# Optimization experiments

Hardware: AMD Instinct MI355X
Metric: run time of the kernel (lower is better)

## Reference

```python
import jax, jax.numpy as jnp
import numpy as np

ALPHA = 1.5
BETA = 0.5
AVG_RATIO = 1.0
SUM_TIMESTEPS = 28000
RANK = 8
K_TOP = RANK * RANK  # k = weight_1_a.shape[1] * weight_2_a.shape[1]


def setup_inputs() -> dict:
    key = jax.random.key(0)
    ks = jax.random.split(key, 5)
    B, S, D_IN, D_OUT = 2, 4096, 4096, 4096
    return {
        "hidden_states": jax.random.normal(ks[0], (B, S, D_IN), dtype=jnp.float32),
        "weight_1_a": jax.random.normal(ks[1], (D_OUT, RANK), dtype=jnp.float32) * 0.02,
        "weight_1_b": jax.random.normal(ks[2], (RANK, D_IN), dtype=jnp.float32) * 0.02,
        "weight_2_a": jax.random.normal(ks[3], (D_OUT, RANK), dtype=jnp.float32) * 0.02,
        "weight_2_b": jax.random.normal(ks[4], (RANK, D_IN), dtype=jnp.float32) * 0.02,
        "timestep": 1,
    }


def reference(hidden_states, weight_1_a, weight_1_b, weight_2_a, weight_2_b, timestep):
    # Low-rank expansions: [out, rank] @ [rank, in] -> [out, in]
    matrix1 = weight_1_a @ weight_1_b
    matrix2 = weight_2_a @ weight_2_b
    top_k_sum1 = jax.lax.top_k(jnp.abs(matrix1).ravel(), K_TOP)[0].sum()
    top_k_sum2 = jax.lax.top_k(jnp.abs(matrix2).ravel(), K_TOP)[0].sum()
    time_ratio = timestep % SUM_TIMESTEPS
    scale = (ALPHA * time_ratio / SUM_TIMESTEPS + BETA) % ALPHA  # pattern 's*'
    temp_ratio = (top_k_sum1 / AVG_RATIO) / (top_k_sum2 * scale)
    weight = jnp.where(temp_ratio > 1.0, matrix1, matrix2)  # [out, in]
    # F.linear: x @ W^T
    return jnp.einsum("bsi,oi->bso", hidden_states, weight)
```

## Files before the change

kernel.cpp:

```cpp
#include <hip/hip_runtime.h>
#include <stdint.h>

#define D 4096
#define RANK 8
#define ALPHA 1.5f
#define BETA 0.5f
#define SUM_TIMESTEPS 28000
#define K_TOP 64
#define NBINS 1024

typedef float f32x4 __attribute__((ext_vector_type(4)));

#define WS_GCNT_OFF 256
#define WS_GSUM_OFF (256 + 2 * NBINS * 4)
#define WS_BMAX_OFF (WS_GSUM_OFF + 2 * NBINS * 8)
#define WS_T_OFF    (WS_BMAX_OFF + 2048)

#define FIX_NUM 2.74877906944e11f
#define FIX_INV 3.637978807091713e-12

__device__ __forceinline__ float dot4v(f32x4 a, f32x4 b) {
    return fmaf(a.x, b.x, fmaf(a.y, b.y, fmaf(a.z, b.z, a.w * b.w)));
}

__global__ __launch_bounds__(256) void k_pass_max(
    const float* __restrict__ wa1, const float* __restrict__ wb1,
    const float* __restrict__ wa2, const float* __restrict__ wb2,
    unsigned* __restrict__ gz, unsigned* __restrict__ bmax) {
    const int tid = threadIdx.x;
    const int mat = blockIdx.y;
    const int bid = blockIdx.x;
    if (mat == 0 && tid < 24) gz[bid * 24 + tid] = 0u;

    const float* __restrict__ wa = mat ? wa2 : wa1;
    const float* __restrict__ wb = mat ? wb2 : wb1;
    const int i0 = (bid & 3) * 1024 + tid * 4;
    const int obase = (bid >> 2) * 64;

    __shared__ float was[64][8];
    if (tid < 128)
        ((f32x4*)was)[tid] = ((const f32x4*)(wa + (size_t)obase * RANK))[tid];

    f32x4 wbv[RANK];
#pragma unroll
    for (int r = 0; r < RANK; ++r)
        wbv[r] = *(const f32x4*)(wb + r * D + i0);
    __syncthreads();

    float vmax = 0.f;
#pragma unroll 4
    for (int oo = 0; oo < 64; ++oo) {
        const f32x4 w03 = *(const f32x4*)&was[oo][0];
        const f32x4 w47 = *(const f32x4*)&was[oo][4];
        f32x4 s = {0.f, 0.f, 0.f, 0.f};
        const float a[8] = {w03.x, w03.y, w03.z, w03.w, w47.x, w47.y, w47.z, w47.w};
#pragma unroll
        for (int r = 0; r < RANK; ++r) {
            s.x = fmaf(a[r], wbv[r].x, s.x);
            s.y = fmaf(a[r], wbv[r].y, s.y);
            s.z = fmaf(a[r], wbv[r].z, s.z);
            s.w = fmaf(a[r], wbv[r].w, s.w);
        }
        vmax = fmaxf(vmax, fmaxf(fmaxf(fabsf(s.x), fabsf(s.y)),
                                 fmaxf(fabsf(s.z), fabsf(s.w))));
    }
    for (int off = 32; off; off >>= 1)
        vmax = fmaxf(vmax, __shfl_xor(vmax, off, 64));
    __shared__ float smax[4];
    const int wave = tid >> 6, lane = tid & 63;
    if (lane == 0) smax[wave] = vmax;
    __syncthreads();
    if (tid == 0) {
        float m = fmaxf(fmaxf(smax[0], smax[1]), fmaxf(smax[2], smax[3]));
        bmax[mat * 256 + bid] = __float_as_uint(m);
    }
}

__device__ __forceinline__ float block_max256(const unsigned* __restrict__ bmax,
                                              int mat, int tid, float* redm) {
    const int wave = tid >> 6, lane = tid & 63;
    float m = 0.f;
    if (tid < 256) m = __uint_as_float(bmax[mat * 256 + tid]);
    for (int off = 32; off; off >>= 1)
        m = fmaxf(m, __shfl_xor(m, off, 64));
    if (tid < 256 && lane == 0) redm[wave] = m;
    __syncthreads();
    return fmaxf(fmaxf(redm[0], redm[1]), fmaxf(redm[2], redm[3]));
}

__global__ __launch_bounds__(256) void k_pass_hist(
    const float* __restrict__ wa1, const float* __restrict__ wb1,
    const float* __restrict__ wa2, const float* __restrict__ wb2,
    const unsigned* __restrict__ bmax,
    unsigned* __restrict__ gcnt, unsigned long long* __restrict__ gsum) {
    __shared__ unsigned lcnt[NBINS];
    __shared__ unsigned long long lsum[NBINS];
    __shared__ float was[64][8];
    __shared__ float redm[4];
    const int tid = threadIdx.x;
    const int mat = blockIdx.y;
    for (int b = tid; b < NBINS; b += 256) { lcnt[b] = 0u; lsum[b] = 0ull; }

    const float* __restrict__ wa = mat ? wa2 : wa1;
    const float* __restrict__ wb = mat ? wb2 : wb1;
    const int i0 = (blockIdx.x & 3) * 1024 + tid * 4;
    const int obase = (blockIdx.x >> 2) * 64;
    if (tid < 128)
        ((f32x4*)was)[tid] = ((const f32x4*)(wa + (size_t)obase * RANK))[tid];

    const float M = block_max256(bmax, mat, tid, redm);
    const float T = 0.5f * M;
    const float fix = FIX_NUM / M;
    const unsigned bitsT = __float_as_uint(T);

    f32x4 wbv[RANK];
#pragma unroll
    for (int r = 0; r < RANK; ++r)
        wbv[r] = *(const f32x4*)(wb + r * D + i0);

#pragma unroll 2
    for (int oo = 0; oo < 64; ++oo) {
        const f32x4 w03 = *(const f32x4*)&was[oo][0];
        const f32x4 w47 = *(const f32x4*)&was[oo][4];
        f32x4 s = {0.f, 0.f, 0.f, 0.f};
        const float a[8] = {w03.x, w03.y, w03.z, w03.w, w47.x, w47.y, w47.z, w47.w};
#pragma unroll
        for (int r = 0; r < RANK; ++r) {
            s.x = fmaf(a[r], wbv[r].x, s.x);
            s.y = fmaf(a[r], wbv[r].y, s.y);
            s.z = fmaf(a[r], wbv[r].z, s.z);
            s.w = fmaf(a[r], wbv[r].w, s.w);
        }
        const float av[4] = {fabsf(s.x), fabsf(s.y), fabsf(s.z), fabsf(s.w)};
#pragma unroll
        for (int j = 0; j < 4; ++j) {
            if (av[j] >= T) {
                unsigned k = (__float_as_uint(av[j]) - bitsT) >> 13;
                if (k > NBINS - 1u) k = NBINS - 1u;
                atomicAdd(&lcnt[k], 1u);
                atomicAdd(&lsum[k], (unsigned long long)(av[j] * fix));
            }
        }
    }
    __syncthreads();
    unsigned* __restrict__ gc = gcnt + (size_t)mat * NBINS;
    unsigned long long* __restrict__ gs = gsum + (size_t)mat * NBINS;
    for (int b = tid; b < NBINS; b += 256) {
        unsigned c = lcnt[b];
        if (c) {
            atomicAdd(&gc[b], c);
            atomicAdd(&gs[b], lsum[b]);
        }
    }
}

__global__ __launch_bounds__(1024) void k_select(
    unsigned* __restrict__ hdr, const unsigned* __restrict__ bmax,
    const unsigned* __restrict__ gcnt, const unsigned long long* __restrict__ gsum,
    const int* __restrict__ tsp) {
    __shared__ unsigned sc[NBINS];
    __shared__ unsigned long long ss[NBINS];
    __shared__ float res[2];
    __shared__ float Ms[2];
    __shared__ float redm[4];
    __shared__ int sB;
    const int b = threadIdx.x;

    for (int mat = 0; mat < 2; ++mat) {
        float M = block_max256(bmax, mat, b, redm);
        if (b == 0) Ms[mat] = M;
        __syncthreads();
    }

    for (int mat = 0; mat < 2; ++mat) {
        if (b == 0) sB = -1;
        const unsigned c0 = gcnt[(size_t)mat * NBINS + b];
        const unsigned long long s0 = gsum[(size_t)mat * NBINS + b];
        __syncthreads();
        sc[b] = c0;
        ss[b] = s0;
        __syncthreads();
        for (int step = 1; step < NBINS; step <<= 1) {
            unsigned c2 = 0u; unsigned long long s2 = 0ull;
            if (b + step < NBINS) { c2 = sc[b + step]; s2 = ss[b + step]; }
            __syncthreads();
            sc[b] += c2;
            ss[b] += s2;
            __syncthreads();
        }
        if (sc[b] >= K_TOP && (b == NBINS - 1 || sc[b + 1] < K_TOP)) sB = b;
        __syncthreads();
        if (b == 0) {
            const double inv = (double)Ms[mat] * FIX_INV;
            float total;
            if (sB < 0) {
                total = (float)((double)ss[0] * inv);
            } else {
                const int B = sB;
                const unsigned cAbove = (B + 1 < NBINS) ? sc[B + 1] : 0u;
                const unsigned long long sAbove = (B + 1 < NBINS) ? ss[B + 1] : 0ull;
                const unsigned cb = sc[B] - cAbove;
                const unsigned long long sb = ss[B] - sAbove;
                const unsigned need = K_TOP - cAbove;
                total = (float)((double)sAbove * inv)
                      + (float)((double)sb * inv) * ((float)need / (float)cb);
            }
            res[mat] = total;
        }
        __syncthreads();
    }
    if (b == 0) {
        const int tr = (*tsp) % SUM_TIMESTEPS;
        const float scale = fmodf(ALPHA * (float)tr / (float)SUM_TIMESTEPS + BETA, ALPHA);
        const float temp_ratio = res[0] / (res[1] * scale);
        hdr[4] = (temp_ratio > 1.0f) ? 1u : 0u;
    }
}

__global__ __launch_bounds__(256) void k_t(
    const float* __restrict__ h,
    const float* __restrict__ wb1, const float* __restrict__ wb2,
    const unsigned* __restrict__ hdr,
    float* __restrict__ t) {
    const int tid = threadIdx.x;
    const int wave = tid >> 6, lane = tid & 63;
    const float* __restrict__ wb = hdr[4] ? wb1 : wb2;
    const size_t m0 = (size_t)blockIdx.x * 8;
    const int r0w = wave * 2;

    __shared__ float wbs[RANK][1024];

    float acc[2][RANK];
#pragma unroll
    for (int row = 0; row < 2; ++row)
#pragma unroll
        for (int r = 0; r < RANK; ++r) acc[row][r] = 0.f;

    const f32x4* __restrict__ src = (const f32x4*)wb;
    f32x4* __restrict__ dst = (f32x4*)wbs;

    for (int q = 0; q < 4; ++q) {
        __syncthreads();
        f32x4 sreg[8];
#pragma unroll
        for (int s = 0; s < 8; ++s) {
            const int j = s * 256 + tid;
            sreg[s] = src[(j >> 8) * 1024 + q * 256 + (j & 255)];
        }
        f32x4 hv[4][2];
#pragma unroll
        for (int k = 0; k < 4; ++k)
#pragma unroll
            for (int row = 0; row < 2; ++row)
                hv[k][row] = *(const f32x4*)(h + (m0 + r0w + row) * D
                                             + q * 1024 + k * 256 + lane * 4);
#pragma unroll
        for (int s = 0; s < 8; ++s) dst[s * 256 + tid] = sreg[s];
        __syncthreads();
#pragma unroll
        for (int k = 0; k < 4; ++k) {
            const int il = k * 256 + lane * 4;
            f32x4 wbv[RANK];
#pragma unroll
            for (int r = 0; r < RANK; ++r)
                wbv[r] = *(const f32x4*)&wbs[r][il];
#pragma unroll
            for (int row = 0; row < 2; ++row)
#pragma unroll
                for (int r = 0; r < RANK; ++r)
                    acc[row][r] = fmaf(hv[k][row].x, wbv[r].x,
                                  fmaf(hv[k][row].y, wbv[r].y,
                                  fmaf(hv[k][row].z, wbv[r].z,
                                  fmaf(hv[k][row].w, wbv[r].w, acc[row][r]))));
        }
    }

#pragma unroll
    for (int row = 0; row < 2; ++row)
#pragma unroll
        for (int r = 0; r < RANK; ++r)
#pragma unroll
            for (int off = 32; off; off >>= 1)
                acc[row][r] += __shfl_xor(acc[row][r], off, 64);
    if (lane == 0) {
#pragma unroll
        for (int row = 0; row < 2; ++row)
#pragma unroll
            for (int r = 0; r < RANK; ++r)
                t[(m0 + r0w + row) * RANK + r] = acc[row][r];
    }
}

__global__ __launch_bounds__(256) void k_o(
    const float* __restrict__ t,
    const float* __restrict__ wa1, const float* __restrict__ wa2,
    const unsigned* __restrict__ hdr,
    float* __restrict__ out) {
    const int tid = threadIdx.x;
    const int wave = tid >> 6, lane = tid & 63;
    const float* __restrict__ wa = hdr[4] ? wa1 : wa2;
    const int cslice = blockIdx.x & 3;
    const size_t m0 = (size_t)(blockIdx.x >> 2) * 32;
    const int o0 = cslice * 1024 + wave * 256 + lane * 4;

    __shared__ float ts[32][8];
    if (tid < 64)
        ((f32x4*)ts)[tid] = *(const f32x4*)(t + m0 * RANK + tid * 4);

    f32x4 A[8];
#pragma unroll
    for (int j = 0; j < 8; ++j)
        A[j] = *(const f32x4*)(wa + (size_t)o0 * RANK + j * 4);
    __syncthreads();

#pragma unroll 4
    for (int row = 0; row < 32; ++row) {
        const f32x4 t03 = *(const f32x4*)&ts[row][0];
        const f32x4 t47 = *(const f32x4*)&ts[row][4];
        f32x4 ov;
        ov.x = dot4v(A[0], t03) + dot4v(A[1], t47);
        ov.y = dot4v(A[2], t03) + dot4v(A[3], t47);
        ov.z = dot4v(A[4], t03) + dot4v(A[5], t47);
        ov.w = dot4v(A[6], t03) + dot4v(A[7], t47);
        __builtin_nontemporal_store(ov, (f32x4*)(out + (m0 + row) * D + o0));
    }
}

extern "C" void kernel_launch(void* const* d_in, const int* in_sizes, int n_in,
                              void* d_out, int out_size, void* d_ws, size_t ws_size,
                              hipStream_t stream) {
    const float* h   = (const float*)d_in[0];
    const float* wa1 = (const float*)d_in[1];
    const float* wb1 = (const float*)d_in[2];
    const float* wa2 = (const float*)d_in[3];
    const float* wb2 = (const float*)d_in[4];
    const int*   ts  = (const int*)d_in[5];
    float* out = (float*)d_out;

    const int rows = in_sizes[0] / D;

    unsigned* hdr  = (unsigned*)d_ws;
    unsigned* gcnt = (unsigned*)((char*)d_ws + WS_GCNT_OFF);
    unsigned long long* gsum = (unsigned long long*)((char*)d_ws + WS_GSUM_OFF);
    unsigned* bmax = (unsigned*)((char*)d_ws + WS_BMAX_OFF);
    float*    tbuf = (float*)((char*)d_ws + WS_T_OFF);

    hipLaunchKernelGGL(k_pass_max, dim3(256, 2), dim3(256), 0, stream,
                       wa1, wb1, wa2, wb2, gcnt, bmax);
    hipLaunchKernelGGL(k_pass_hist, dim3(256, 2), dim3(256), 0, stream,
                       wa1, wb1, wa2, wb2, bmax, gcnt, gsum);
    hipLaunchKernelGGL(k_select, dim3(1), dim3(1024), 0, stream,
                       hdr, bmax, gcnt, gsum, ts);
    hipLaunchKernelGGL(k_t, dim3(rows / 8), dim3(256), 0, stream,
                       h, wb1, wb2, hdr, tbuf);
    hipLaunchKernelGGL(k_o, dim3(4 * (rows / 32)), dim3(256), 0, stream,
                       tbuf, wa1, wa2, hdr, out);
}
```

Before: 94.18 us.

## Split k_t reduction across K chunks with partial sums reduced in k_o

The hidden_states x W_b^T projection kernel now gives each wave one 256-wide K chunk for two rows and writes per-chunk partial sums, where before each block looped over the full K with shared-memory staging of W_b. The consumer kernel k_o sums the 16 partials per row when it loads its t tile. This is meant to raise parallelism (16x more waves) and drop the LDS staging and barriers, so the 128 MB read of h streams at higher bandwidth. In exchange W_b is re-read from global/L2 by every wave, the workspace grows for the partial buffer, and k_o does extra strided reads.

Result: slower. 135.3 us (+43.7%).

```diff
diff --git a/kernel.cpp b/kernel.cpp
--- a/kernel.cpp
+++ b/kernel.cpp
@@ -14,7 +14,7 @@
 #define WS_GCNT_OFF 256
 #define WS_GSUM_OFF (256 + 2 * NBINS * 4)
 #define WS_BMAX_OFF (WS_GSUM_OFF + 2 * NBINS * 8)
-#define WS_T_OFF    (WS_BMAX_OFF + 2048)
+#define WS_PART_OFF (WS_BMAX_OFF + 2048)
 
 #define FIX_NUM 2.74877906944e11f
 #define FIX_INV 3.637978807091713e-12
@@ -221,78 +221,50 @@
     const float* __restrict__ h,
     const float* __restrict__ wb1, const float* __restrict__ wb2,
     const unsigned* __restrict__ hdr,
-    float* __restrict__ t) {
+    float* __restrict__ part) {
     const int tid = threadIdx.x;
-    const int wave = tid >> 6, lane = tid & 63;
+    const int lane = tid & 63;
     const float* __restrict__ wb = hdr[4] ? wb1 : wb2;
-    const size_t m0 = (size_t)blockIdx.x * 8;
-    const int r0w = wave * 2;
-
-    __shared__ float wbs[RANK][1024];
-
-    float acc[2][RANK];
-#pragma unroll
-    for (int row = 0; row < 2; ++row)
-#pragma unroll
-        for (int r = 0; r < RANK; ++r) acc[row][r] = 0.f;
-
-    const f32x4* __restrict__ src = (const f32x4*)wb;
-    f32x4* __restrict__ dst = (f32x4*)wbs;
-
-    for (int q = 0; q < 4; ++q) {
-        __syncthreads();
-        f32x4 sreg[8];
-#pragma unroll
-        for (int s = 0; s < 8; ++s) {
-            const int j = s * 256 + tid;
-            sreg[s] = src[(j >> 8) * 1024 + q * 256 + (j & 255)];
-        }
-        f32x4 hv[4][2];
-#pragma unroll
-        for (int k = 0; k < 4; ++k)
-#pragma unroll
-            for (int row = 0; row < 2; ++row)
-                hv[k][row] = *(const f32x4*)(h + (m0 + r0w + row) * D
-                                             + q * 1024 + k * 256 + lane * 4);
-#pragma unroll
-        for (int s = 0; s < 8; ++s) dst[s * 256 + tid] = sreg[s];
-        __syncthreads();
-#pragma unroll
-        for (int k = 0; k < 4; ++k) {
-            const int il = k * 256 + lane * 4;
-            f32x4 wbv[RANK];
-#pragma unroll
-            for (int r = 0; r < RANK; ++r)
-                wbv[r] = *(const f32x4*)&wbs[r][il];
-#pragma unroll
-            for (int row = 0; row < 2; ++row)
-#pragma unroll
-                for (int r = 0; r < RANK; ++r)
-                    acc[row][r] = fmaf(hv[k][row].x, wbv[r].x,
-                                  fmaf(hv[k][row].y, wbv[r].y,
-                                  fmaf(hv[k][row].z, wbv[r].z,
-                                  fmaf(hv[k][row].w, wbv[r].w, acc[row][r]))));
-        }
-    }
-
-#pragma unroll
-    for (int row = 0; row < 2; ++row)
-#pragma unroll
-        for (int r = 0; r < RANK; ++r)
-#pragma unroll
-            for (int off = 32; off; off >>= 1)
-                acc[row][r] += __shfl_xor(acc[row][r], off, 64);
+    const int wg = blockIdx.x * 4 + (tid >> 6);
+    const int mp = wg >> 4;
+    const int w  = wg & 15;
+    const size_t m = (size_t)mp * 2;
+    const int i0 = w * 256 + lane * 4;
+
+    const f32x4 h0 = *(const f32x4*)(h + m * D + i0);
+    const f32x4 h1 = *(const f32x4*)(h + (m + 1) * D + i0);
+    f32x4 wbv[RANK];
+#pragma unroll
+    for (int r = 0; r < RANK; ++r)
+        wbv[r] = *(const f32x4*)(wb + r * D + i0);
+
+    float acc[16];
+#pragma unroll
+    for (int r = 0; r < RANK; ++r) {
+        acc[r]     = dot4v(h0, wbv[r]);
+        acc[8 + r] = dot4v(h1, wbv[r]);
+    }
+#pragma unroll
+    for (int off = 32; off; off >>= 1)
+#pragma unroll
+        for (int j = 0; j < 16; ++j)
+            acc[j] += __shfl_xor(acc[j], off, 64);
+
     if (lane == 0) {
-#pragma unroll
-        for (int row = 0; row < 2; ++row)
-#pragma unroll
-            for (int r = 0; r < RANK; ++r)
-                t[(m0 + r0w + row) * RANK + r] = acc[row][r];
+        float* __restrict__ dst = part + (size_t)wg * 16;
+        const f32x4 v0 = {acc[0], acc[1], acc[2], acc[3]};
+        const f32x4 v1 = {acc[4], acc[5], acc[6], acc[7]};
+        const f32x4 v2 = {acc[8], acc[9], acc[10], acc[11]};
+        const f32x4 v3 = {acc[12], acc[13], acc[14], acc[15]};
+        *(f32x4*)(dst)      = v0;
+        *(f32x4*)(dst + 4)  = v1;
+        *(f32x4*)(dst + 8)  = v2;
+        *(f32x4*)(dst + 12) = v3;
     }
 }
 
 __global__ __launch_bounds__(256) void k_o(
-    const float* __restrict__ t,
+    const float* __restrict__ part,
     const float* __restrict__ wa1, const float* __restrict__ wa2,
     const unsigned* __restrict__ hdr,
     float* __restrict__ out) {
@@ -304,8 +276,16 @@
     const int o0 = cslice * 1024 + wave * 256 + lane * 4;
 
     __shared__ float ts[32][8];
-    if (tid < 64)
-        ((f32x4*)ts)[tid] = *(const f32x4*)(t + m0 * RANK + tid * 4);
+    {
+        const int row = tid >> 3, r = tid & 7;
+        const size_t mp = (m0 >> 1) + (row >> 1);
+        const int half = (row & 1) * 8;
+        const float* __restrict__ p = part + (mp * 16) * 16 + half + r;
+        float s = 0.f;
+#pragma unroll
+        for (int w = 0; w < 16; ++w) s += p[w * 16];
+        ts[row][r] = s;
+    }
 
     f32x4 A[8];
 #pragma unroll
@@ -343,7 +323,7 @@
     unsigned* gcnt = (unsigned*)((char*)d_ws + WS_GCNT_OFF);
     unsigned long long* gsum = (unsigned long long*)((char*)d_ws + WS_GSUM_OFF);
     unsigned* bmax = (unsigned*)((char*)d_ws + WS_BMAX_OFF);
-    float*    tbuf = (float*)((char*)d_ws + WS_T_OFF);
+    float*    part = (float*)((char*)d_ws + WS_PART_OFF);
 
     hipLaunchKernelGGL(k_pass_max, dim3(256, 2), dim3(256), 0, stream,
                        wa1, wb1, wa2, wb2, gcnt, bmax);
@@ -351,8 +331,8 @@
                        wa1, wb1, wa2, wb2, bmax, gcnt, gsum);
     hipLaunchKernelGGL(k_select, dim3(1), dim3(1024), 0, stream,
                        hdr, bmax, gcnt, gsum, ts);
-    hipLaunchKernelGGL(k_t, dim3(rows / 8), dim3(256), 0, stream,
-                       h, wb1, wb2, hdr, tbuf);
+    hipLaunchKernelGGL(k_t, dim3((rows / 2) * 16 / 4), dim3(256), 0, stream,
+                       h, wb1, wb2, hdr, part);
     hipLaunchKernelGGL(k_o, dim3(4 * (rows / 32)), dim3(256), 0, stream,
-                       tbuf, wa1, wa2, hdr, out);
-}
+                       part, wa1, wa2, hdr, out);
+}
```

## Load full wb into LDS once per 1024-thread block in k_t

Applied to the files above, without the earlier changes.

k_t now uses 1024-thread blocks that each handle 32 rows. The whole 128KB rank-8 wb matrix is staged into dynamic LDS once per block, replacing four chunked reload phases with barriers. Each block now re-reads wb from L2 for 32 rows instead of 8, but the large LDS footprint limits occupancy to one block per CU. The t writes become vectorized, and k_o drops its nontemporal output stores in favour of plain stores.

New measurement: 107.7 us. +14.3%, slower.

```diff
diff --git a/kernel.cpp b/kernel.cpp
--- a/kernel.cpp
+++ b/kernel.cpp
@@ -217,18 +217,26 @@
     }
 }
 
-__global__ __launch_bounds__(256) void k_t(
+__global__ __launch_bounds__(1024) void k_t(
     const float* __restrict__ h,
     const float* __restrict__ wb1, const float* __restrict__ wb2,
     const unsigned* __restrict__ hdr,
     float* __restrict__ t) {
+    extern __shared__ float wbs[];
     const int tid = threadIdx.x;
     const int wave = tid >> 6, lane = tid & 63;
     const float* __restrict__ wb = hdr[4] ? wb1 : wb2;
-    const size_t m0 = (size_t)blockIdx.x * 8;
-    const int r0w = wave * 2;
-
-    __shared__ float wbs[RANK][1024];
+
+    {
+        const f32x4* __restrict__ src = (const f32x4*)wb;
+        f32x4* __restrict__ dst = (f32x4*)wbs;
+#pragma unroll
+        for (int s = 0; s < 8; ++s)
+            dst[s * 1024 + tid] = src[s * 1024 + tid];
+    }
+    __syncthreads();
+
+    const size_t m0 = (size_t)blockIdx.x * 32 + wave * 2;
 
     float acc[2][RANK];
 #pragma unroll
@@ -236,42 +244,21 @@
 #pragma unroll
         for (int r = 0; r < RANK; ++r) acc[row][r] = 0.f;
 
-    const f32x4* __restrict__ src = (const f32x4*)wb;
-    f32x4* __restrict__ dst = (f32x4*)wbs;
-
-    for (int q = 0; q < 4; ++q) {
-        __syncthreads();
-        f32x4 sreg[8];
-#pragma unroll
-        for (int s = 0; s < 8; ++s) {
-            const int j = s * 256 + tid;
-            sreg[s] = src[(j >> 8) * 1024 + q * 256 + (j & 255)];
-        }
-        f32x4 hv[4][2];
-#pragma unroll
-        for (int k = 0; k < 4; ++k)
-#pragma unroll
-            for (int row = 0; row < 2; ++row)
-                hv[k][row] = *(const f32x4*)(h + (m0 + r0w + row) * D
-                                             + q * 1024 + k * 256 + lane * 4);
-#pragma unroll
-        for (int s = 0; s < 8; ++s) dst[s * 256 + tid] = sreg[s];
-        __syncthreads();
-#pragma unroll
-        for (int k = 0; k < 4; ++k) {
-            const int il = k * 256 + lane * 4;
-            f32x4 wbv[RANK];
-#pragma unroll
-            for (int r = 0; r < RANK; ++r)
-                wbv[r] = *(const f32x4*)&wbs[r][il];
-#pragma unroll
-            for (int row = 0; row < 2; ++row)
-#pragma unroll
-                for (int r = 0; r < RANK; ++r)
-                    acc[row][r] = fmaf(hv[k][row].x, wbv[r].x,
-                                  fmaf(hv[k][row].y, wbv[r].y,
-                                  fmaf(hv[k][row].z, wbv[r].z,
-                                  fmaf(hv[k][row].w, wbv[r].w, acc[row][r]))));
+#pragma unroll 2
+    for (int k = 0; k < 16; ++k) {
+        const int i = k * 256 + lane * 4;
+        const f32x4 h0 = *(const f32x4*)(h + m0 * D + i);
+        const f32x4 h1 = *(const f32x4*)(h + (m0 + 1) * D + i);
+        f32x4 wbv[RANK];
+#pragma unroll
+        for (int r = 0; r < RANK; ++r)
+            wbv[r] = *(const f32x4*)&wbs[r * D + i];
+#pragma unroll
+        for (int r = 0; r < RANK; ++r) {
+            acc[0][r] = fmaf(h0.x, wbv[r].x, fmaf(h0.y, wbv[r].y,
+                        fmaf(h0.z, wbv[r].z, fmaf(h0.w, wbv[r].w, acc[0][r]))));
+            acc[1][r] = fmaf(h1.x, wbv[r].x, fmaf(h1.y, wbv[r].y,
+                        fmaf(h1.z, wbv[r].z, fmaf(h1.w, wbv[r].w, acc[1][r]))));
         }
     }
 
@@ -283,11 +270,12 @@
             for (int off = 32; off; off >>= 1)
                 acc[row][r] += __shfl_xor(acc[row][r], off, 64);
     if (lane == 0) {
-#pragma unroll
-        for (int row = 0; row < 2; ++row)
-#pragma unroll
-            for (int r = 0; r < RANK; ++r)
-                t[(m0 + r0w + row) * RANK + r] = acc[row][r];
+        const f32x4 v0 = {acc[0][0], acc[0][1], acc[0][2], acc[0][3]};
+        const f32x4 v1 = {acc[0][4], acc[0][5], acc[0][6], acc[0][7]};
+        const f32x4 v2 = {acc[1][0], acc[1][1], acc[1][2], acc[1][3]};
+        const f32x4 v3 = {acc[1][4], acc[1][5], acc[1][6], acc[1][7]};
+        f32x4* __restrict__ dst = (f32x4*)(t + m0 * RANK);
+        dst[0] = v0; dst[1] = v1; dst[2] = v2; dst[3] = v3;
     }
 }
 
@@ -322,7 +310,7 @@
         ov.y = dot4v(A[2], t03) + dot4v(A[3], t47);
         ov.z = dot4v(A[4], t03) + dot4v(A[5], t47);
         ov.w = dot4v(A[6], t03) + dot4v(A[7], t47);
-        __builtin_nontemporal_store(ov, (f32x4*)(out + (m0 + row) * D + o0));
+        *(f32x4*)(out + (m0 + row) * D + o0) = ov;
     }
 }
 
@@ -345,13 +333,18 @@
     unsigned* bmax = (unsigned*)((char*)d_ws + WS_BMAX_OFF);
     float*    tbuf = (float*)((char*)d_ws + WS_T_OFF);
 
+    (void)hipFuncSetAttribute((const void*)k_t,
+                              hipFuncAttributeMaxDynamicSharedMemorySize,
+                              RANK * D * (int)sizeof(float));
+
     hipLaunchKernelGGL(k_pass_max, dim3(256, 2), dim3(256), 0, stream,
                        wa1, wb1, wa2, wb2, gcnt, bmax);
     hipLaunchKernelGGL(k_pass_hist, dim3(256, 2), dim3(256), 0, stream,
                        wa1, wb1, wa2, wb2, bmax, gcnt, gsum);
     hipLaunchKernelGGL(k_select, dim3(1), dim3(1024), 0, stream,
                        hdr, bmax, gcnt, gsum, ts);
-    hipLaunchKernelGGL(k_t, dim3(rows / 8), dim3(256), 0, stream,
+    hipLaunchKernelGGL(k_t, dim3(rows / 32), dim3(1024),
+                       RANK * D * sizeof(float), stream,
                        h, wb1, wb2, hdr, tbuf);
     hipLaunchKernelGGL(k_o, dim3(4 * (rows / 32)), dim3(256), 0, stream,
                        tbuf, wa1, wa2, hdr, out);
```
